# Kernel optimization log

Measured on AMD Instinct MI355X. Metric: run time of the kernel, lower is better.

## Reference

```python
import jax, jax.numpy as jnp
import numpy as np

N, D = 16384, 128

def setup_inputs() -> dict:
    key = jax.random.key(0)
    k1, k2 = jax.random.split(key)
    x = jax.random.normal(k1, (N, D), dtype=jnp.float32)
    adj = jax.random.randint(k2, (N, N), 0, 2, dtype=jnp.int32)
    return {"x": x, "adj": adj}

def reference(x, adj):
    # out[i] = x[i] + sum_{j: adj[i,j]==1} x[j]  ==  (adj + I) @ x
    a = adj.astype(x.dtype)
    return x + jnp.matmul(a, x)  # [N, D]
```

## Files before the change

### kernel.cpp

```cpp
#include <hip/hip_runtime.h>
#include <hip/hip_bf16.h>

#define GN 16384
#define GD 128
#define KSPLIT 4
#define KBLK (GN / KSPLIT)
#define BK 64
#define NPER (KBLK / BK)
#define BUF_SHORTS (GD * BK)
#define OUT_ELEMS (GN * GD)

typedef __attribute__((ext_vector_type(8))) short short8;
typedef __attribute__((ext_vector_type(4))) float floatx4;
typedef __attribute__((ext_vector_type(4))) int intx4;

static __device__ __forceinline__ unsigned short f32_to_bf16(float f) {
  unsigned u = __builtin_bit_cast(unsigned, f);
  unsigned r = u + 0x7FFFu + ((u >> 16) & 1u);
  return (unsigned short)(r >> 16);
}

__global__ __launch_bounds__(256) void prep_kernel(const float* __restrict__ x,
                                                   unsigned short* __restrict__ xT) {
  __shared__ unsigned short t[GD][66];
  const int tid = threadIdx.x;
  const int j0 = blockIdx.x * 64;
  for (int i = tid; i < 64 * GD; i += 256) {
    int j = i >> 7, d = i & (GD - 1);
    t[d][j] = f32_to_bf16(x[(size_t)(j0 + j) * GD + d]);
  }
  __syncthreads();
  for (int i = tid; i < GD * 32; i += 256) {
    int d = i >> 5, jp = i & 31;
    unsigned lo = t[d][2 * jp], hi = t[d][2 * jp + 1];
    *reinterpret_cast<unsigned*>(xT + (size_t)d * GN + j0 + 2 * jp) = lo | (hi << 16);
  }
}

__global__ __launch_bounds__(256, 4) void gemm_kernel(const int* __restrict__ adj,
                                                      const unsigned short* __restrict__ xT,
                                                      float* __restrict__ partials) {
  __shared__ unsigned short bbuf[2][BUF_SHORTS];
  const int tid = threadIdx.x;
  const int wave = tid >> 6;
  const int lane = tid & 63;
  const int q = lane >> 4;
  const int m = lane & 15;
  const int rbase = blockIdx.x * 64 + wave * 16;
  const int ks = blockIdx.y;
  const int kbase = ks * KBLK;

  const unsigned short* gptr[4];
  unsigned short* lptr[4];
#pragma unroll
  for (int p = 0; p < 4; ++p) {
    int s = tid + 256 * p;
    int n = s >> 3;
    int gsrc = (s & 7) ^ (n & 7);
    gptr[p] = xT + (size_t)n * GN + kbase + gsrc * 8;
    lptr[p] = &bbuf[0][0] + (size_t)s * 8;
  }

#define STAGE(bufsel, koff)                                                             \
  do {                                                                                  \
    _Pragma("unroll") for (int p = 0; p < 4; ++p) {                                     \
      __builtin_amdgcn_global_load_lds(                                                 \
          (const __attribute__((address_space(1))) unsigned int*)(gptr[p] + (koff)),    \
          (__attribute__((address_space(3))) unsigned int*)(lptr[p] +                   \
                                                           (bufsel) * BUF_SHORTS),      \
          16, 0, 0);                                                                    \
    }                                                                                   \
  } while (0)

  const int* a0 = adj + (size_t)(rbase + m) * GN + kbase + q * 8;

  floatx4 acc[8];
#pragma unroll
  for (int c = 0; c < 8; ++c) acc[c] = (floatx4){0.f, 0.f, 0.f, 0.f};

  STAGE(0, 0);
  intx4 ca[4];
  ca[0] = __builtin_nontemporal_load((const intx4*)(a0));
  ca[1] = __builtin_nontemporal_load((const intx4*)(a0 + 4));
  ca[2] = __builtin_nontemporal_load((const intx4*)(a0 + 32));
  ca[3] = __builtin_nontemporal_load((const intx4*)(a0 + 36));

  int buf = 0;
  for (int c = 0; c < NPER; ++c) {
    __syncthreads();
    const int nk = ((c + 1) & (NPER - 1)) * BK;
    if (c + 1 < NPER) STAGE(buf ^ 1, nk);
    intx4 na[4];
    na[0] = __builtin_nontemporal_load((const intx4*)(a0 + nk));
    na[1] = __builtin_nontemporal_load((const intx4*)(a0 + nk + 4));
    na[2] = __builtin_nontemporal_load((const intx4*)(a0 + nk + 32));
    na[3] = __builtin_nontemporal_load((const intx4*)(a0 + nk + 36));

#pragma unroll
    for (int kk = 0; kk < 2; ++kk) {
      short8 bf[8];
      const unsigned short* bb = &bbuf[buf][0] + ((4 * kk + q) ^ (m & 7)) * 8;
#pragma unroll
      for (int cc = 0; cc < 8; ++cc)
        bf[cc] = *(const short8*)(bb + (cc * 16 + m) * BK);

      const intx4 r0 = ca[2 * kk], r1 = ca[2 * kk + 1];
      intx4 pk;
      pk.x = (r0.x | (r0.y << 16)) * 0x3F80;
      pk.y = (r0.z | (r0.w << 16)) * 0x3F80;
      pk.z = (r1.x | (r1.y << 16)) * 0x3F80;
      pk.w = (r1.z | (r1.w << 16)) * 0x3F80;
      const short8 af = __builtin_bit_cast(short8, pk);

#pragma unroll
      for (int cc = 0; cc < 8; ++cc)
        acc[cc] = __builtin_amdgcn_mfma_f32_16x16x32_bf16(af, bf[cc], acc[cc], 0, 0, 0);
    }

#pragma unroll
    for (int u = 0; u < 4; ++u) ca[u] = na[u];
    buf ^= 1;
  }

  float* pp = partials + (size_t)ks * OUT_ELEMS + (size_t)rbase * GD;
#pragma unroll
  for (int cc = 0; cc < 8; ++cc)
#pragma unroll
    for (int r = 0; r < 4; ++r)
      pp[(size_t)(q * 4 + r) * GD + cc * 16 + m] = acc[cc][r];
}

__global__ __launch_bounds__(256) void reduce_kernel(const float* __restrict__ x,
                                                     const float* __restrict__ partials,
                                                     float* __restrict__ out) {
  size_t i = ((size_t)blockIdx.x * 256 + threadIdx.x) * 4;
  floatx4 v = *(const floatx4*)(x + i);
  v += *(const floatx4*)(partials + 0 * (size_t)OUT_ELEMS + i);
  v += *(const floatx4*)(partials + 1 * (size_t)OUT_ELEMS + i);
  v += *(const floatx4*)(partials + 2 * (size_t)OUT_ELEMS + i);
  v += *(const floatx4*)(partials + 3 * (size_t)OUT_ELEMS + i);
  *(floatx4*)(out + i) = v;
}

extern "C" void kernel_launch(void* const* d_in, const int* in_sizes, int n_in,
                              void* d_out, int out_size, void* d_ws, size_t ws_size,
                              hipStream_t stream) {
  const float* x = (const float*)d_in[0];
  const int* adj = (const int*)d_in[1];
  float* out = (float*)d_out;
  unsigned short* xT = (unsigned short*)d_ws;
  float* partials = (float*)((char*)d_ws + (size_t)GN * GD * 2);

  prep_kernel<<<GN / 64, 256, 0, stream>>>(x, xT);
  gemm_kernel<<<dim3(GN / 64, KSPLIT), 256, 0, stream>>>(adj, xT, partials);
  reduce_kernel<<<OUT_ELEMS / 4 / 256, 256, 0, stream>>>(x, partials, out);
}
```

Baseline: 1.373 ms.

## Enlarge GEMM block to 8 waves and 128-wide K phases sharing staged B tile

Blocks now hold 512 threads (8 waves, 128 rows) and stage a 128-deep K slice of the transposed x tile into LDS per phase, halving the number of block syncs and doubling reuse of each staged B tile across waves. The adjacency prefetch moves to a finer per-32 step software pipeline and uses regular loads instead of nontemporal loads. LDS use per block doubles to 64KB, which may limit resident blocks per CU, and dropping nontemporal hints may change cache behaviour for the streamed adjacency matrix.

Result: no change. 1.349 ms (-1.7%).

```diff
diff --git a/kernel.cpp b/kernel.cpp
--- a/kernel.cpp
+++ b/kernel.cpp
@@ -5,9 +5,10 @@
 #define GD 128
 #define KSPLIT 4
 #define KBLK (GN / KSPLIT)
-#define BK 64
-#define NPER (KBLK / BK)
-#define BUF_SHORTS (GD * BK)
+#define PHK 128
+#define NPH (KBLK / PHK)
+#define NSTEP (PHK / 32)
+#define BUF_SHORTS (GD * PHK)
 #define OUT_ELEMS (GN * GD)
 
 typedef __attribute__((ext_vector_type(8))) short short8;
@@ -37,7 +38,7 @@
   }
 }
 
-__global__ __launch_bounds__(256, 4) void gemm_kernel(const int* __restrict__ adj,
+__global__ __launch_bounds__(512, 4) void gemm_kernel(const int* __restrict__ adj,
                                                       const unsigned short* __restrict__ xT,
                                                       float* __restrict__ partials) {
   __shared__ unsigned short bbuf[2][BUF_SHORTS];
@@ -46,7 +47,7 @@
   const int lane = tid & 63;
   const int q = lane >> 4;
   const int m = lane & 15;
-  const int rbase = blockIdx.x * 64 + wave * 16;
+  const int rbase = blockIdx.x * 128 + wave * 16;
   const int ks = blockIdx.y;
   const int kbase = ks * KBLK;
 
@@ -54,9 +55,9 @@
   unsigned short* lptr[4];
 #pragma unroll
   for (int p = 0; p < 4; ++p) {
-    int s = tid + 256 * p;
-    int n = s >> 3;
-    int gsrc = (s & 7) ^ (n & 7);
+    int s = tid + 512 * p;
+    int n = s >> 4;
+    int gsrc = (s & 15) ^ (n & 7);
     gptr[p] = xT + (size_t)n * GN + kbase + gsrc * 8;
     lptr[p] = &bbuf[0][0] + (size_t)s * 8;
   }
@@ -79,46 +80,41 @@
   for (int c = 0; c < 8; ++c) acc[c] = (floatx4){0.f, 0.f, 0.f, 0.f};
 
   STAGE(0, 0);
-  intx4 ca[4];
-  ca[0] = __builtin_nontemporal_load((const intx4*)(a0));
-  ca[1] = __builtin_nontemporal_load((const intx4*)(a0 + 4));
-  ca[2] = __builtin_nontemporal_load((const intx4*)(a0 + 32));
-  ca[3] = __builtin_nontemporal_load((const intx4*)(a0 + 36));
+  intx4 ca0 = *(const intx4*)(a0);
+  intx4 ca1 = *(const intx4*)(a0 + 4);
 
   int buf = 0;
-  for (int c = 0; c < NPER; ++c) {
+  for (int ph = 0; ph < NPH; ++ph) {
     __syncthreads();
-    const int nk = ((c + 1) & (NPER - 1)) * BK;
-    if (c + 1 < NPER) STAGE(buf ^ 1, nk);
-    intx4 na[4];
-    na[0] = __builtin_nontemporal_load((const intx4*)(a0 + nk));
-    na[1] = __builtin_nontemporal_load((const intx4*)(a0 + nk + 4));
-    na[2] = __builtin_nontemporal_load((const intx4*)(a0 + nk + 32));
-    na[3] = __builtin_nontemporal_load((const intx4*)(a0 + nk + 36));
+    if (ph + 1 < NPH) STAGE(buf ^ 1, (ph + 1) * PHK);
 
 #pragma unroll
-    for (int kk = 0; kk < 2; ++kk) {
+    for (int st = 0; st < NSTEP; ++st) {
+      const int g = ph * NSTEP + st;
+      const int nk = ((g + 1) & (KBLK / 32 - 1)) * 32;
+      intx4 na0 = *(const intx4*)(a0 + nk);
+      intx4 na1 = *(const intx4*)(a0 + nk + 4);
+
       short8 bf[8];
-      const unsigned short* bb = &bbuf[buf][0] + ((4 * kk + q) ^ (m & 7)) * 8;
+      const unsigned short* bb = &bbuf[buf][0] + (((st * 4 + q) ^ (m & 7)) * 8);
 #pragma unroll
       for (int cc = 0; cc < 8; ++cc)
-        bf[cc] = *(const short8*)(bb + (cc * 16 + m) * BK);
+        bf[cc] = *(const short8*)(bb + (cc * 16 + m) * PHK);
 
-      const intx4 r0 = ca[2 * kk], r1 = ca[2 * kk + 1];
       intx4 pk;
-      pk.x = (r0.x | (r0.y << 16)) * 0x3F80;
-      pk.y = (r0.z | (r0.w << 16)) * 0x3F80;
-      pk.z = (r1.x | (r1.y << 16)) * 0x3F80;
-      pk.w = (r1.z | (r1.w << 16)) * 0x3F80;
+      pk.x = (ca0.x | (ca0.y << 16)) * 0x3F80;
+      pk.y = (ca0.z | (ca0.w << 16)) * 0x3F80;
+      pk.z = (ca1.x | (ca1.y << 16)) * 0x3F80;
+      pk.w = (ca1.z | (ca1.w << 16)) * 0x3F80;
       const short8 af = __builtin_bit_cast(short8, pk);
 
 #pragma unroll
       for (int cc = 0; cc < 8; ++cc)
         acc[cc] = __builtin_amdgcn_mfma_f32_16x16x32_bf16(af, bf[cc], acc[cc], 0, 0, 0);
+
+      ca0 = na0;
+      ca1 = na1;
     }
-
-#pragma unroll
-    for (int u = 0; u < 4; ++u) ca[u] = na[u];
     buf ^= 1;
   }
 
@@ -152,6 +148,6 @@
   float* partials = (float*)((char*)d_ws + (size_t)GN * GD * 2);
 
   prep_kernel<<<GN / 64, 256, 0, stream>>>(x, xT);
-  gemm_kernel<<<dim3(GN / 64, KSPLIT), 256, 0, stream>>>(adj, xT, partials);
+  gemm_kernel<<<dim3(GN / 128, KSPLIT), 512, 0, stream>>>(adj, xT, partials);
   reduce_kernel<<<OUT_ELEMS / 4 / 256, 256, 0, stream>>>(x, partials, out);
 }
```
